# Performance work log

Hardware: AMD Instinct MI355X
Metric: run time of the kernel (lower is better)

The kernel has to match this reference:

```python
import jax, jax.numpy as jnp
import numpy as np

T = 1.0
N_NEG = 50
NUM_CLASSES = 500  # smoothing denominator K from CrossEntropyLabelSmooth (faithful quirk)
EPS = 0.1

B, C, D = 2048, 65536, 256


def setup_inputs() -> dict:
    key = jax.random.key(0)
    k1, k2, k3 = jax.random.split(key, 3)
    f = jax.random.normal(k1, (B, D), dtype=jnp.float32)
    centers = jax.random.normal(k2, (C, D), dtype=jnp.float32)
    label = jax.random.randint(k3, (B,), 0, C, dtype=jnp.int64)
    return {"f": f, "centers": centers, "label": label}


def reference(f, centers, label):
    b = f.shape[0]
    rows = jnp.arange(b)
    mat = f @ centers.T                              # [B, C] similarity scores
    pos = mat[rows, label][:, None]                  # [B, 1] positive score
    # mask the positive column so top-k picks only negatives
    masked = mat.at[rows, label].set(-jnp.inf)
    neg, _ = jax.lax.top_k(masked, N_NEG)            # [B, N_neg]
    preds = jnp.concatenate([pos, neg], axis=1) / T  # [B, 1 + N_neg]
    log_probs = jax.nn.log_softmax(preds, axis=1)
    # label-smoothed one-hot with target class 0 (the positive)
    onehot = jnp.zeros_like(log_probs).at[:, 0].set(1.0)
    targets = (1.0 - EPS) * onehot + EPS / NUM_CLASSES
    loss = (-targets * log_probs).mean(0).sum()
    return loss
```

## Files before the change

kernel.cpp:

```cpp
#include <hip/hip_runtime.h>
#include <hip/hip_fp16.h>

#define B_ROWS 2048
#define C_COLS 65536
#define D_DIM  256
#define N_NEG  50
#define NTILES (C_COLS / 128)
#define SN 136

typedef __attribute__((ext_vector_type(8))) short short8;
typedef __attribute__((ext_vector_type(4))) float floatx4;
typedef __fp16 f16x2 __attribute__((ext_vector_type(2)));
typedef __fp16 h8v  __attribute__((ext_vector_type(8)));
typedef __fp16 h4v  __attribute__((ext_vector_type(4)));
typedef __fp16 h2v  __attribute__((ext_vector_type(2)));

__device__ __forceinline__ ushort f2bf(float f) {
  unsigned u = __float_as_uint(f);
  unsigned r = (u + 0x7FFFu + ((u >> 16) & 1u)) >> 16;
  return (ushort)r;
}

__global__ void cvt_both(const float* __restrict__ f, const float* __restrict__ cen,
                         ushort* __restrict__ fb, ushort* __restrict__ cb, int doCen) {
  int i = blockIdx.x * blockDim.x + threadIdx.x;
  int row = i >> 5;
  int ka = i & 31, ktile = ka >> 3, kb = ka & 7;
  const float* src; ushort* dst; int r;
  if (row < B_ROWS) { src = f; dst = fb; r = row; }
  else { if (!doCen) return; src = cen; dst = cb; r = row - B_ROWS; }
  const float4* s = (const float4*)(src + (size_t)r * D_DIM + ka * 8);
  float4 a = s[0], b = s[1];
  uint4 o;
  o.x = (uint)f2bf(a.x) | ((uint)f2bf(a.y) << 16);
  o.y = (uint)f2bf(a.z) | ((uint)f2bf(a.w) << 16);
  o.z = (uint)f2bf(b.x) | ((uint)f2bf(b.y) << 16);
  o.w = (uint)f2bf(b.z) | ((uint)f2bf(b.w) << 16);
  *(uint4*)(dst + (size_t)r * D_DIM + ktile * 64 + ((kb ^ (r & 7)) << 3)) = o;
}

__device__ __forceinline__ void async16(const void* g, void* l) {
  __builtin_amdgcn_global_load_lds((const __attribute__((address_space(1))) void*)g,
                                   (__attribute__((address_space(3))) void*)l,
                                   16, 0, 0);
}

template <bool PREB>
__global__ void gemm_reduce(const ushort* __restrict__ fb,
                            const ushort* __restrict__ cb,
                            const float* __restrict__ cen,
                            const int* __restrict__ label,
                            float* __restrict__ cand) {
  __shared__ __align__(16) char smem[SN * 128 * 2];
  __shared__ int labLDS[128];
  ushort* Cs = (ushort*)smem;
  ushort* Fs = Cs + 8192;
  ushort* scu = (ushort*)smem;

  const int tid = threadIdx.x, wave = tid >> 6, lane = tid & 63;
  const int l = lane & 15, q = lane >> 4;
  const int m0 = blockIdx.x * 128, n0 = blockIdx.y * 128;
  const int bxTile = blockIdx.y;
  if (tid < 128) labLDS[tid] = label[m0 + tid];

  floatx4 acc[4][4] = {};
  const int wn = (wave >> 1) * 64, wm = (wave & 1) * 64;

  for (int kt = 0; kt < D_DIM / 64; ++kt) {
#pragma unroll
    for (int r = 0; r < 4; ++r) {
      int idx = r * 2048 + wave * 512 + lane * 8;
      int row = idx >> 6, kk = idx & 63;
      async16(fb + (size_t)(m0 + row) * D_DIM + kt * 64 + kk, Fs + r * 2048 + wave * 512);
      if (PREB)
        async16(cb + (size_t)(n0 + row) * D_DIM + kt * 64 + kk, Cs + r * 2048 + wave * 512);
    }
    if (!PREB) {
#pragma unroll
      for (int g = 0; g < 4; ++g) {
        int e = (tid + g * 256) * 8;
        int row = e >> 6, kblk = (e >> 3) & 7;
        const float* gp = cen + (size_t)(n0 + row) * D_DIM + kt * 64 + kblk * 8;
        float4 fa = *(const float4*)gp;
        float4 fbv = *(const float4*)(gp + 4);
        uint4 o;
        o.x = (uint)f2bf(fa.x)  | ((uint)f2bf(fa.y)  << 16);
        o.y = (uint)f2bf(fa.z)  | ((uint)f2bf(fa.w)  << 16);
        o.z = (uint)f2bf(fbv.x) | ((uint)f2bf(fbv.y) << 16);
        o.w = (uint)f2bf(fbv.z) | ((uint)f2bf(fbv.w) << 16);
        *(uint4*)(Cs + (row << 6) + ((kblk ^ (row & 7)) << 3)) = o;
      }
    }
    __syncthreads();

#pragma unroll
    for (int ks = 0; ks < 2; ++ks) {
      short8 a[4], b[4];
#pragma unroll
      for (int i = 0; i < 4; ++i) {
        int swz = ((4 * ks + q) ^ (l & 7)) << 3;
        a[i] = *(const short8*)(Cs + ((wn + i * 16 + l) << 6) + swz);
        b[i] = *(const short8*)(Fs + ((wm + i * 16 + l) << 6) + swz);
      }
#pragma unroll
      for (int i = 0; i < 4; ++i)
#pragma unroll
        for (int j = 0; j < 4; ++j)
          acc[i][j] = __builtin_amdgcn_mfma_f32_16x16x32_bf16(a[i], b[j], acc[i][j], 0, 0, 0);
    }
    __syncthreads();
  }

  __half* sc = (__half*)scu;
#pragma unroll
  for (int i = 0; i < 4; ++i)
#pragma unroll
    for (int j = 0; j < 4; ++j) {
      int mloc = wm + j * 16 + l;
      int nloc = wn + i * 16 + q * 4;
      f16x2 h0 = __builtin_amdgcn_cvt_pkrtz(acc[i][j][0], acc[i][j][1]);
      f16x2 h1 = __builtin_amdgcn_cvt_pkrtz(acc[i][j][2], acc[i][j][3]);
      uint2 w;
      w.x = *(const uint*)&h0;
      w.y = *(const uint*)&h1;
      *(uint2*)(sc + mloc * SN + nloc) = w;
    }
  __syncthreads();

  {
    const int r = tid >> 1, hf = tid & 1;
    const ushort* bp = scu + r * SN + hf * 64;
    const int rel = labLDS[r] - (n0 + hf * 64);
    if ((unsigned)rel < 64u) ((ushort*)bp)[rel] = 0xFC00;
    h8v v0 = ((const h8v*)bp)[0], v1 = ((const h8v*)bp)[1];
    h8v v2 = ((const h8v*)bp)[2], v3 = ((const h8v*)bp)[3];
    h8v v4 = ((const h8v*)bp)[4], v5 = ((const h8v*)bp)[5];
    h8v v6 = ((const h8v*)bp)[6], v7 = ((const h8v*)bp)[7];
    h8v m8 = __builtin_elementwise_max(
        __builtin_elementwise_max(__builtin_elementwise_max(v0, v1), __builtin_elementwise_max(v2, v3)),
        __builtin_elementwise_max(__builtin_elementwise_max(v4, v5), __builtin_elementwise_max(v6, v7)));
    h4v m4 = __builtin_elementwise_max(m8.lo, m8.hi);
    h2v m2 = __builtin_elementwise_max(m4.lo, m4.hi);
    float outv = fmaxf((float)m2.x, (float)m2.y);
    cand[(size_t)(m0 + r) * (NTILES * 2) + bxTile * 2 + hf] = outv;
  }
}

__device__ __forceinline__ float dec_key(int k) {
  if (k < 0x0400) return -INFINITY;
  ushort h = (k >= 0x8000) ? (ushort)(k ^ 0x8000) : (ushort)(~k & 0xFFFF);
  __half_raw hr; hr.x = h;
  return __half2float((__half)hr);
}

__global__ void final_select(const float* __restrict__ cand, const float* __restrict__ f,
                             const float* __restrict__ cen, const int* __restrict__ label,
                             float* __restrict__ out) {
  __shared__ float sred[8];
  __shared__ int   sint[8];
  const int row = blockIdx.x, tid = threadIdx.x;
  const int lane = tid & 63, wid = tid >> 6;
  const int lab = label[row];

  float4 u = ((const float4*)(cand + (size_t)row * (NTILES * 2)))[tid];
  float v[4] = {u.x, u.y, u.z, u.w};
  float pv = f[(size_t)row * D_DIM + tid] * cen[(size_t)lab * D_DIM + tid];
  float m = fmaxf(fmaxf(v[0], v[1]), fmaxf(v[2], v[3]));
#pragma unroll
  for (int o = 32; o > 0; o >>= 1) {
    m = fmaxf(m, __shfl_down(m, o));
    pv += __shfl_down(pv, o);
  }
  if (lane == 0) { sred[wid] = m; sred[4 + wid] = pv; }
  __syncthreads();
  m = fmaxf(fmaxf(sred[0], sred[1]), fmaxf(sred[2], sred[3]));
  const float pos = sred[4] + sred[5] + sred[6] + sred[7];

  __half hm = __float2half(m);
  int hb = (int)(*(ushort*)&hm);
  int km = (m >= 0.f) ? (0x8000 | hb) : (~hb & 0xFFFF);
  int lo = km - 2048, hi = km;
  if (lo < 0x0400) lo = 0x0400;
#pragma unroll
  for (int it = 0; it < 12; ++it) {
    int mid = (lo + hi) >> 1;
    float tau = dec_key(mid);
    int c = (v[0] > tau) + (v[1] > tau) + (v[2] > tau) + (v[3] > tau);
#pragma unroll
    for (int o = 32; o > 0; o >>= 1) c += __shfl_down(c, o);
    if (lane == 0) sint[(it & 1) * 4 + wid] = c;
    __syncthreads();
    int base = (it & 1) * 4;
    int tot = sint[base] + sint[base + 1] + sint[base + 2] + sint[base + 3];
    if (tot <= 49) hi = mid; else lo = mid + 1;
  }

  const float tau = dec_key(hi);
  float sum = 0.f, se = 0.f; int c = 0;
#pragma unroll
  for (int k = 0; k < 4; ++k) {
    if (v[k] > tau) { ++c; sum += v[k]; se += expf(v[k] - m); }
  }
#pragma unroll
  for (int o = 32; o > 0; o >>= 1) {
    sum += __shfl_down(sum, o);
    se  += __shfl_down(se, o);
    c   += __shfl_down(c, o);
  }
  if (lane == 0) { sred[wid] = sum; sred[4 + wid] = se; sint[wid] = c; }
  __syncthreads();
  if (tid == 0) {
    float S = sred[0] + sred[1] + sred[2] + sred[3];
    float E = sred[4] + sred[5] + sred[6] + sred[7];
    int   C = sint[0] + sint[1] + sint[2] + sint[3];
    float nfill = (float)(N_NEG - C);
    S += nfill * tau;
    E += nfill * expf(tau - m);
    float M = fmaxf(m, pos);
    float seAll = E * expf(m - M) + expf(pos - M);
    float lse = M + logf(seAll);
    float loss = 0.9102f * lse - 0.9002f * pos - 2.0e-4f * S;
    atomicAdd(out, loss * (1.0f / B_ROWS));
  }
}

extern "C" void kernel_launch(void* const* d_in, const int* in_sizes, int n_in,
                              void* d_out, int out_size, void* d_ws, size_t ws_size,
                              hipStream_t stream) {
  const float* f   = (const float*)d_in[0];
  const float* cen = (const float*)d_in[1];
  const int*   label = (const int*)d_in[2];
  float* out = (float*)d_out;

  char* ws = (char*)d_ws;
  float*  cand = (float*)ws;
  ushort* fb   = (ushort*)(ws + 8388608);
  ushort* cb   = (ushort*)(ws + 9437184);
  const bool pre = ws_size >= (9437184ull + 33554432ull);

  hipMemsetAsync(d_out, 0, out_size * sizeof(float), stream);

  cvt_both<<<(B_ROWS + C_COLS) / 8, 256, 0, stream>>>(f, cen, fb, cb, pre ? 1 : 0);

  dim3 grid(B_ROWS / 128, NTILES);
  if (pre) {
    gemm_reduce<true><<<grid, 256, 0, stream>>>(fb, cb, cen, label, cand);
  } else {
    gemm_reduce<false><<<grid, 256, 0, stream>>>(fb, nullptr, cen, label, cand);
  }

  final_select<<<B_ROWS, 256, 0, stream>>>(cand, f, cen, label, out);
}
```

Baseline: 214.3 us.

## Pre-swizzle bf16 operands into MFMA fragment order and reduce maxima in registers

The conversion kernel now writes f and centers in bf16, already arranged in the per-lane MFMA fragment order. The GEMM then loads the centers operand straight from global memory into registers, and only the f slab goes through LDS, in two halves. The masked max reduction now runs on the fp32 accumulators with cross-lane shuffles instead of an fp16 LDS scratch tile, and launch bounds ask for three blocks per CU. This drops the LDS staging for one operand and the LDS epilogue round trip. In exchange, centers loads are no longer shared through LDS within the block, the fallback path for a small workspace is removed, and the code assumes the workspace is always large enough.

```diff
diff --git a/kernel.cpp b/kernel.cpp
--- a/kernel.cpp
+++ b/kernel.cpp
@@ -6,37 +6,41 @@
 #define D_DIM  256
 #define N_NEG  50
 #define NTILES (C_COLS / 128)
-#define SN 136
 
 typedef __attribute__((ext_vector_type(8))) short short8;
 typedef __attribute__((ext_vector_type(4))) float floatx4;
-typedef __fp16 f16x2 __attribute__((ext_vector_type(2)));
-typedef __fp16 h8v  __attribute__((ext_vector_type(8)));
-typedef __fp16 h4v  __attribute__((ext_vector_type(4)));
-typedef __fp16 h2v  __attribute__((ext_vector_type(2)));
-
-__device__ __forceinline__ ushort f2bf(float f) {
+
+__device__ __forceinline__ uint f2bf(float f) {
   unsigned u = __float_as_uint(f);
-  unsigned r = (u + 0x7FFFu + ((u >> 16) & 1u)) >> 16;
-  return (ushort)r;
-}
-
-__global__ void cvt_both(const float* __restrict__ f, const float* __restrict__ cen,
-                         ushort* __restrict__ fb, ushort* __restrict__ cb, int doCen) {
-  int i = blockIdx.x * blockDim.x + threadIdx.x;
-  int row = i >> 5;
-  int ka = i & 31, ktile = ka >> 3, kb = ka & 7;
-  const float* src; ushort* dst; int r;
-  if (row < B_ROWS) { src = f; dst = fb; r = row; }
-  else { if (!doCen) return; src = cen; dst = cb; r = row - B_ROWS; }
-  const float4* s = (const float4*)(src + (size_t)r * D_DIM + ka * 8);
+  return (u + 0x7FFFu + ((u >> 16) & 1u)) >> 16;
+}
+
+__global__ void cvt_frag(const float* __restrict__ f, const float* __restrict__ cen,
+                         ushort* __restrict__ fF, ushort* __restrict__ cbF) {
+  int c = blockIdx.x * blockDim.x + threadIdx.x;
+  const float* src; ushort* dst; int row, k;
+  if (c < 65536) {
+    int l = c & 15, qq = (c >> 4) & 3, ks = (c >> 6) & 1, ktl = (c >> 7) & 1;
+    int j8 = (c >> 8) & 7, h2 = (c >> 11) & 1, slab = c >> 12;
+    row = slab * 128 + j8 * 16 + l;
+    k = (h2 * 2 + ktl) * 64 + ks * 32 + qq * 8;
+    src = f; dst = fF + (size_t)c * 8;
+  } else {
+    int c2 = c - 65536;
+    int l = c2 & 15, qq = (c2 >> 4) & 3, ks = (c2 >> 6) & 1, kt = (c2 >> 7) & 3;
+    int i8 = (c2 >> 9) & 7, t = c2 >> 12;
+    row = t * 128 + i8 * 16 + l;
+    k = kt * 64 + ks * 32 + qq * 8;
+    src = cen; dst = cbF + (size_t)c2 * 8;
+  }
+  const float4* s = (const float4*)(src + (size_t)row * D_DIM + k);
   float4 a = s[0], b = s[1];
   uint4 o;
-  o.x = (uint)f2bf(a.x) | ((uint)f2bf(a.y) << 16);
-  o.y = (uint)f2bf(a.z) | ((uint)f2bf(a.w) << 16);
-  o.z = (uint)f2bf(b.x) | ((uint)f2bf(b.y) << 16);
-  o.w = (uint)f2bf(b.z) | ((uint)f2bf(b.w) << 16);
-  *(uint4*)(dst + (size_t)r * D_DIM + ktile * 64 + ((kb ^ (r & 7)) << 3)) = o;
+  o.x = f2bf(a.x) | (f2bf(a.y) << 16);
+  o.y = f2bf(a.z) | (f2bf(a.w) << 16);
+  o.z = f2bf(b.x) | (f2bf(b.y) << 16);
+  o.w = f2bf(b.z) | (f2bf(b.w) << 16);
+  *(uint4*)dst = o;
 }
 
 __device__ __forceinline__ void async16(const void* g, void* l) {
@@ -45,105 +49,71 @@
                                    16, 0, 0);
 }
 
-template <bool PREB>
-__global__ void gemm_reduce(const ushort* __restrict__ fb,
-                            const ushort* __restrict__ cb,
-                            const float* __restrict__ cen,
-                            const int* __restrict__ label,
-                            float* __restrict__ cand) {
-  __shared__ __align__(16) char smem[SN * 128 * 2];
-  __shared__ int labLDS[128];
-  ushort* Cs = (ushort*)smem;
-  ushort* Fs = Cs + 8192;
-  ushort* scu = (ushort*)smem;
-
+__global__ __launch_bounds__(256, 3)
+void gemm_frag(const ushort* __restrict__ fF, const ushort* __restrict__ cbF,
+               const int* __restrict__ label, float* __restrict__ cand) {
+  __shared__ __align__(16) ushort Fs[16384];
   const int tid = threadIdx.x, wave = tid >> 6, lane = tid & 63;
   const int l = lane & 15, q = lane >> 4;
-  const int m0 = blockIdx.x * 128, n0 = blockIdx.y * 128;
-  const int bxTile = blockIdx.y;
-  if (tid < 128) labLDS[tid] = label[m0 + tid];
+  const int slab = blockIdx.x, t = blockIdx.y;
+  const int m0 = slab * 128, n0 = t * 128;
+  const int wn = (wave >> 1) * 64, wm = (wave & 1) * 64;
 
   floatx4 acc[4][4] = {};
-  const int wn = (wave >> 1) * 64, wm = (wave & 1) * 64;
-
-  for (int kt = 0; kt < D_DIM / 64; ++kt) {
-#pragma unroll
-    for (int r = 0; r < 4; ++r) {
-      int idx = r * 2048 + wave * 512 + lane * 8;
-      int row = idx >> 6, kk = idx & 63;
-      async16(fb + (size_t)(m0 + row) * D_DIM + kt * 64 + kk, Fs + r * 2048 + wave * 512);
-      if (PREB)
-        async16(cb + (size_t)(n0 + row) * D_DIM + kt * 64 + kk, Cs + r * 2048 + wave * 512);
+  const ushort* aBase = cbF + ((size_t)(t * 8 + (wn >> 4)) * 8) * 512 + lane * 8;
+
+#pragma unroll
+  for (int h2 = 0; h2 < 2; ++h2) {
+    if (h2) __syncthreads();
+    const ushort* src = fF + ((size_t)(slab * 2 + h2)) * 16384;
+#pragma unroll
+    for (int r = 0; r < 8; ++r)
+      async16(src + r * 2048 + wave * 512 + lane * 8, Fs + r * 2048 + wave * 512);
+    __syncthreads();
+
+#pragma unroll
+    for (int ktl = 0; ktl < 2; ++ktl)
+#pragma unroll
+      for (int ks = 0; ks < 2; ++ks) {
+        const int kt = h2 * 2 + ktl;
+        short8 a[4], b[4];
+#pragma unroll
+        for (int i = 0; i < 4; ++i)
+          a[i] = *(const short8*)(aBase + i * 4096 + kt * 1024 + ks * 512);
+#pragma unroll
+        for (int j = 0; j < 4; ++j)
+          b[j] = *(const short8*)(Fs + (((((wm >> 4) + j) * 2 + ktl) * 2 + ks) * 64 + lane) * 8);
+#pragma unroll
+        for (int i = 0; i < 4; ++i)
+#pragma unroll
+          for (int j = 0; j < 4; ++j)
+            acc[i][j] = __builtin_amdgcn_mfma_f32_16x16x32_bf16(a[i], b[j], acc[i][j], 0, 0, 0);
+      }
+  }
+
+  float gm[4];
+#pragma unroll
+  for (int j = 0; j < 4; ++j) {
+    const int lab = label[m0 + wm + j * 16 + l];
+    const int rel = lab - (n0 + wn);
+    if ((unsigned)rel < 64u && ((rel >> 2) & 3) == q) {
+      const int ii = rel >> 4, rr = rel & 3;
+#pragma unroll
+      for (int i = 0; i < 4; ++i)
+#pragma unroll
+        for (int r = 0; r < 4; ++r)
+          if (i == ii && r == rr) acc[i][j][r] = -INFINITY;
     }
-    if (!PREB) {
-#pragma unroll
-      for (int g = 0; g < 4; ++g) {
-        int e = (tid + g * 256) * 8;
-        int row = e >> 6, kblk = (e >> 3) & 7;
-        const float* gp = cen + (size_t)(n0 + row) * D_DIM + kt * 64 + kblk * 8;
-        float4 fa = *(const float4*)gp;
-        float4 fbv = *(const float4*)(gp + 4);
-        uint4 o;
-        o.x = (uint)f2bf(fa.x)  | ((uint)f2bf(fa.y)  << 16);
-        o.y = (uint)f2bf(fa.z)  | ((uint)f2bf(fa.w)  << 16);
-        o.z = (uint)f2bf(fbv.x) | ((uint)f2bf(fbv.y) << 16);
-        o.w = (uint)f2bf(fbv.z) | ((uint)f2bf(fbv.w) << 16);
-        *(uint4*)(Cs + (row << 6) + ((kblk ^ (row & 7)) << 3)) = o;
-      }
-    }
-    __syncthreads();
-
-#pragma unroll
-    for (int ks = 0; ks < 2; ++ks) {
-      short8 a[4], b[4];
-#pragma unroll
-      for (int i = 0; i < 4; ++i) {
-        int swz = ((4 * ks + q) ^ (l & 7)) << 3;
-        a[i] = *(const short8*)(Cs + ((wn + i * 16 + l) << 6) + swz);
-        b[i] = *(const short8*)(Fs + ((wm + i * 16 + l) << 6) + swz);
-      }
-#pragma unroll
-      for (int i = 0; i < 4; ++i)
-#pragma unroll
-        for (int j = 0; j < 4; ++j)
-          acc[i][j] = __builtin_amdgcn_mfma_f32_16x16x32_bf16(a[i], b[j], acc[i][j], 0, 0, 0);
-    }
-    __syncthreads();
-  }
-
-  __half* sc = (__half*)scu;
-#pragma unroll
-  for (int i = 0; i < 4; ++i)
-#pragma unroll
-    for (int j = 0; j < 4; ++j) {
-      int mloc = wm + j * 16 + l;
-      int nloc = wn + i * 16 + q * 4;
-      f16x2 h0 = __builtin_amdgcn_cvt_pkrtz(acc[i][j][0], acc[i][j][1]);
-      f16x2 h1 = __builtin_amdgcn_cvt_pkrtz(acc[i][j][2], acc[i][j][3]);
-      uint2 w;
-      w.x = *(const uint*)&h0;
-      w.y = *(const uint*)&h1;
-      *(uint2*)(sc + mloc * SN + nloc) = w;
-    }
-  __syncthreads();
-
-  {
-    const int r = tid >> 1, hf = tid & 1;
-    const ushort* bp = scu + r * SN + hf * 64;
-    const int rel = labLDS[r] - (n0 + hf * 64);
-    if ((unsigned)rel < 64u) ((ushort*)bp)[rel] = 0xFC00;
-    h8v v0 = ((const h8v*)bp)[0], v1 = ((const h8v*)bp)[1];
-    h8v v2 = ((const h8v*)bp)[2], v3 = ((const h8v*)bp)[3];
-    h8v v4 = ((const h8v*)bp)[4], v5 = ((const h8v*)bp)[5];
-    h8v v6 = ((const h8v*)bp)[6], v7 = ((const h8v*)bp)[7];
-    h8v m8 = __builtin_elementwise_max(
-        __builtin_elementwise_max(__builtin_elementwise_max(v0, v1), __builtin_elementwise_max(v2, v3)),
-        __builtin_elementwise_max(__builtin_elementwise_max(v4, v5), __builtin_elementwise_max(v6, v7)));
-    h4v m4 = __builtin_elementwise_max(m8.lo, m8.hi);
-    h2v m2 = __builtin_elementwise_max(m4.lo, m4.hi);
-    float outv = fmaxf((float)m2.x, (float)m2.y);
-    cand[(size_t)(m0 + r) * (NTILES * 2) + bxTile * 2 + hf] = outv;
-  }
+    float v = -INFINITY;
+#pragma unroll
+    for (int i = 0; i < 4; ++i)
+      v = fmaxf(v, fmaxf(fmaxf(acc[i][j][0], acc[i][j][1]), fmaxf(acc[i][j][2], acc[i][j][3])));
+    v = fmaxf(v, __shfl_xor(v, 16));
+    v = fmaxf(v, __shfl_xor(v, 32));
+    gm[j] = v;
+  }
+  float outv = (q == 0) ? gm[0] : (q == 1) ? gm[1] : (q == 2) ? gm[2] : gm[3];
+  cand[(size_t)(m0 + wm + lane) * (NTILES * 2) + t * 2 + (wn >> 6)] = outv;
 }
 
 __device__ __forceinline__ float dec_key(int k) {
@@ -234,20 +204,15 @@
 
   char* ws = (char*)d_ws;
   float*  cand = (float*)ws;
-  ushort* fb   = (ushort*)(ws + 8388608);
-  ushort* cb   = (ushort*)(ws + 9437184);
-  const bool pre = ws_size >= (9437184ull + 33554432ull);
+  ushort* fF   = (ushort*)(ws + 8388608);
+  ushort* cbF  = (ushort*)(ws + 9437184);
 
   hipMemsetAsync(d_out, 0, out_size * sizeof(float), stream);
 
-  cvt_both<<<(B_ROWS + C_COLS) / 8, 256, 0, stream>>>(f, cen, fb, cb, pre ? 1 : 0);
+  cvt_frag<<<(65536 + 2097152) / 256, 256, 0, stream>>>(f, cen, fF, cbF);
 
   dim3 grid(B_ROWS / 128, NTILES);
-  if (pre) {
-    gemm_reduce<true><<<grid, 256, 0, stream>>>(fb, cb, cen, label, cand);
-  } else {
-    gemm_reduce<false><<<grid, 256, 0, stream>>>(fb, nullptr, cen, label, cand);
-  }
+  gemm_frag<<<grid, 256, 0, stream>>>(fF, cbF, label, cand);
 
   final_select<<<B_ROWS, 256, 0, stream>>>(cand, f, cen, label, out);
 }
```

Result: no change. 211.1 us (-1.5%).
